# Kernel tuning notes

Measured on AMD Instinct MI355X. Metric: run time of the kernel, lower is better.

## Reference

```python
import jax, jax.numpy as jnp
import numpy as np

NEG_INF = -1e30


def setup_inputs() -> dict:
    key = jax.random.key(0)
    k1, k2, k3 = jax.random.split(key, 3)
    B, d, Lc, Lq = 64, 128, 1024, 256
    C = jax.random.normal(k1, (B, d, Lc), dtype=jnp.float32)
    Q = jax.random.normal(k2, (B, d, Lq), dtype=jnp.float32)
    cmask = jnp.ones((B, Lc), dtype=jnp.float32)
    qmask = jnp.ones((B, Lq), dtype=jnp.float32)
    # trilinear weight, uniform(-sqrt(1/d), sqrt(1/d)) as in the module init
    lim = float(np.sqrt(1.0 / d))
    w = jax.random.uniform(k3, (3 * d,), dtype=jnp.float32, minval=-lim, maxval=lim)
    return {"C": C, "Q": Q, "cmask": cmask, "qmask": qmask, "w": w}


def reference(C, Q, cmask, qmask, w):
    # C: (B, d, Lc), Q: (B, d, Lq) -> channel-last
    Ct = jnp.swapaxes(C, 1, 2)  # (B, Lc, d)
    Qt = jnp.swapaxes(Q, 1, 2)  # (B, Lq, d)
    d = Ct.shape[-1]
    w1, w2, w3 = w[:d], w[d:2 * d], w[2 * d:]
    # Decomposed trilinear score: S[b,i,j] = Ct[b,i].w1 + Qt[b,j].w2 + (Ct[b,i]*w3).Qt[b,j]
    S = (Ct @ w1)[:, :, None] + (Qt @ w2)[:, None, :] \
        + jnp.einsum('bid,bjd->bij', Ct * w3, Qt)  # (B, Lc, Lq)
    qm = qmask[:, None, :]  # (B, 1, Lq)
    cm = cmask[:, :, None]  # (B, Lc, 1)
    S1 = jax.nn.softmax(S + (1.0 - qm) * NEG_INF, axis=2)  # over query
    S2 = jax.nn.softmax(S + (1.0 - cm) * NEG_INF, axis=1)  # over context
    A = jnp.einsum('bij,bjd->bid', S1, Qt)                  # (B, Lc, d)
    Bmat = jnp.einsum('bik,bkd->bid',
                      jnp.einsum('bij,bkj->bik', S1, S2), Ct)  # (B, Lc, d)
    out = jnp.concatenate([Ct, A, Ct * A, Ct * Bmat], axis=2)  # (B, Lc, 4d)
    # dropout in eval mode (p applied only in training) -> identity
    return jnp.swapaxes(out, 1, 2)  # (B, 4d, Lc)
```

## Files before the change

kernel.cpp:

```cpp
#include <hip/hip_runtime.h>
#include <math.h>

#define B_ 64
#define D_ 128
#define LC 1024
#define LQ 256
#define NEG_INF_ (-1e30f)
#define NSPLIT 8

typedef short bf16x8 __attribute__((ext_vector_type(8)));
typedef float f32x4 __attribute__((ext_vector_type(4)));
typedef _Float16 f16x8 __attribute__((ext_vector_type(8)));
typedef _Float16 f16x4 __attribute__((ext_vector_type(4)));

__device__ __forceinline__ unsigned short bf16b(float x) {
  unsigned u = __builtin_bit_cast(unsigned, x);
  u = (u + 0x7FFFu + ((u >> 16) & 1u)) >> 16;
  return (unsigned short)u;
}

__global__ __launch_bounds__(256) void k_ca(const float* __restrict__ C,
                                            const float* __restrict__ w,
                                            float* __restrict__ ca) {
  int t = blockIdx.x * 256 + threadIdx.x;
  int b = t >> 10, i = t & (LC - 1);
  const float* Cp = C + (size_t)b * D_ * LC + i;
  float acc = 0.f;
#pragma unroll 8
  for (int dd = 0; dd < D_; ++dd) acc += Cp[(size_t)dd * LC] * w[dd];
  ca[t] = acc;
}

__global__ __launch_bounds__(256) void k_qb(const float* __restrict__ Q,
                                            const float* __restrict__ w,
                                            float* __restrict__ qb) {
  int t = blockIdx.x * 256 + threadIdx.x;
  int b = t >> 8, j = t & (LQ - 1);
  const float* Qp = Q + (size_t)b * D_ * LQ + j;
  float acc = 0.f;
#pragma unroll 8
  for (int dd = 0; dd < D_; ++dd) acc += Qp[(size_t)dd * LQ] * w[D_ + dd];
  qb[t] = acc;
}

__global__ __launch_bounds__(256) void k_qt(const float* __restrict__ Q,
                                            unsigned short* __restrict__ Qt) {
  __shared__ float ts[64][65];
  int b = blockIdx.z, d0 = blockIdx.y * 64, j0 = blockIdx.x * 64;
  int t = threadIdx.x;
  int jc = t & 15, dr = t >> 4;
#pragma unroll
  for (int ii = 0; ii < 4; ++ii) {
    int d = dr + 16 * ii;
    float4 v = *(const float4*)&Q[((size_t)b * D_ + d0 + d) * LQ + j0 + 4 * jc];
    ts[4 * jc + 0][d] = v.x;
    ts[4 * jc + 1][d] = v.y;
    ts[4 * jc + 2][d] = v.z;
    ts[4 * jc + 3][d] = v.w;
  }
  __syncthreads();
  int j = t >> 2, h = t & 3;
  unsigned short tmp[16];
#pragma unroll
  for (int k = 0; k < 16; ++k) tmp[k] = bf16b(ts[j][h * 16 + k]);
  size_t base = ((size_t)b * LQ + j0 + j) * D_ + d0 + h * 16;
  *(bf16x8*)&Qt[base] = *(bf16x8*)&tmp[0];
  *(bf16x8*)&Qt[base + 8] = *(bf16x8*)&tmp[8];
}

__global__ __launch_bounds__(256, 3) void k_S(const float* __restrict__ C,
                                              const unsigned short* __restrict__ Qt,
                                              const float* __restrict__ w,
                                              const float* __restrict__ ca,
                                              const float* __restrict__ qb,
                                              const float* __restrict__ qmask,
                                              _Float16* __restrict__ S,
                                              float* __restrict__ m1,
                                              float* __restrict__ l1) {
  __shared__ unsigned short Asw[64 * 128];
  int b = blockIdx.y;
  int i0 = blockIdx.x * 64;
  int t = threadIdx.x;
  {
    int fc = t & 15, dr = t >> 4;
#pragma unroll
    for (int ii = 0; ii < 8; ++ii) {
      int d = dr + 16 * ii;
      float w3 = w[2 * D_ + d];
      float4 v = *(const float4*)&C[((size_t)b * D_ + d) * LC + i0 + 4 * fc];
      float vv[4] = {v.x, v.y, v.z, v.w};
#pragma unroll
      for (int m = 0; m < 4; ++m) {
        int i = 4 * fc + m;
        Asw[i * 128 + (d ^ ((i & 7) << 3))] = bf16b(vv[m] * w3);
      }
    }
  }
  __syncthreads();

  int w_id = t >> 6, l = t & 63;
  int sl = l >> 4, lj = l & 15;
  int irow = w_id * 16 + lj;
  f32x4 acc[16];
#pragma unroll
  for (int jt = 0; jt < 16; ++jt) acc[jt] = (f32x4){0.f, 0.f, 0.f, 0.f};

#pragma unroll
  for (int kk = 0; kk < 4; ++kk) {
    bf16x8 af = *(const bf16x8*)&Asw[irow * 128 + ((kk * 32 + 8 * sl) ^ ((irow & 7) << 3))];
#pragma unroll
    for (int jt = 0; jt < 16; ++jt) {
      bf16x8 bf = *(const bf16x8*)&Qt[((size_t)b * LQ + jt * 16 + lj) * D_ + kk * 32 + 8 * sl];
      acc[jt] = __builtin_amdgcn_mfma_f32_16x16x32_bf16(af, bf, acc[jt], 0, 0, 0);
    }
  }

  int ibase = i0 + w_id * 16 + 4 * sl;
  float4 cav = *(const float4*)&ca[b * LC + ibase];
  float cavr[4] = {cav.x, cav.y, cav.z, cav.w};
#pragma unroll
  for (int jt = 0; jt < 16; ++jt) {
    int j = jt * 16 + lj;
    float qbv = qb[b * LQ + j];
    float qadd = (1.0f - qmask[b * LQ + j]) * NEG_INF_;
#pragma unroll
    for (int r = 0; r < 4; ++r) {
      float sval = acc[jt][r] + cavr[r] + qbv;
      S[((size_t)(b * LC + ibase + r)) * LQ + j] = (_Float16)sval;
      acc[jt][r] = sval + qadd;
    }
  }
#pragma unroll
  for (int r = 0; r < 4; ++r) {
    float m = -1e38f;
#pragma unroll
    for (int jt = 0; jt < 16; ++jt) m = fmaxf(m, acc[jt][r]);
#pragma unroll
    for (int off = 1; off <= 8; off <<= 1) m = fmaxf(m, __shfl_xor(m, off));
    float s = 0.f;
#pragma unroll
    for (int jt = 0; jt < 16; ++jt) s += __expf(acc[jt][r] - m);
#pragma unroll
    for (int off = 1; off <= 8; off <<= 1) s += __shfl_xor(s, off);
    if (lj == 0) {
      m1[b * LC + ibase + r] = m;
      l1[b * LC + ibase + r] = s;
    }
  }
}

__global__ __launch_bounds__(256) void k_colpart(const _Float16* __restrict__ S,
                                                 const float* __restrict__ cmask,
                                                 float* __restrict__ pm,
                                                 float* __restrict__ pl) {
  int split = blockIdx.x, b = blockIdx.y;
  int j = threadIdx.x;
  int ibeg = split * (LC / NSPLIT);
  float m = -1e38f, lsum = 0.f;
  for (int i = ibeg; i < ibeg + LC / NSPLIT; ++i) {
    float cm = cmask[b * LC + i];
    float v = (float)S[((size_t)b * LC + i) * LQ + j] + (1.0f - cm) * NEG_INF_;
    float nm = fmaxf(m, v);
    lsum = lsum * __expf(m - nm) + __expf(v - nm);
    m = nm;
  }
  pm[((size_t)b * NSPLIT + split) * LQ + j] = m;
  pl[((size_t)b * NSPLIT + split) * LQ + j] = lsum;
}

__global__ __launch_bounds__(256) void k_colfin(const float* __restrict__ pm,
                                                const float* __restrict__ pl,
                                                float* __restrict__ m2,
                                                float* __restrict__ l2) {
  int t = blockIdx.x * 256 + threadIdx.x;
  int b = t >> 8, j = t & (LQ - 1);
  float m = -1e38f;
#pragma unroll
  for (int s = 0; s < NSPLIT; ++s) m = fmaxf(m, pm[((size_t)b * NSPLIT + s) * LQ + j]);
  float lsum = 0.f;
#pragma unroll
  for (int s = 0; s < NSPLIT; ++s)
    lsum += pl[((size_t)b * NSPLIT + s) * LQ + j] * __expf(pm[((size_t)b * NSPLIT + s) * LQ + j] - m);
  m2[t] = m;
  l2[t] = lsum;
}

__global__ __launch_bounds__(256, 4) void k_R(const _Float16* __restrict__ S,
                                              const float* __restrict__ C,
                                              const float* __restrict__ cmask,
                                              const float* __restrict__ m2,
                                              const float* __restrict__ l2,
                                              unsigned short* __restrict__ Rt) {
  __shared__ unsigned short Pt[2][32 * 32];
  __shared__ float m2s[32], il2s[32];
  int b = blockIdx.y;
  int j0 = blockIdx.x * 32;
  int t = threadIdx.x;
  if (t < 32) {
    m2s[t] = m2[b * LQ + j0 + t];
    il2s[t] = 1.0f / l2[b * LQ + j0 + t];
  }
  __syncthreads();

  int iL = t >> 3, jc = t & 7;
  int w_id = t >> 6, l = t & 63;
  int sl = l >> 4, lj = l & 15;
  int wbase = w_id * 32;

  f32x4 acc[2][2];
#pragma unroll
  for (int dt = 0; dt < 2; ++dt)
#pragma unroll
    for (int jt = 0; jt < 2; ++jt) acc[dt][jt] = (f32x4){0.f, 0.f, 0.f, 0.f};

  {
    f16x4 sv = *(const f16x4*)&S[((size_t)(b * LC + iL)) * LQ + j0 + 4 * jc];
    float cmadd = (1.0f - cmask[b * LC + iL]) * NEG_INF_;
#pragma unroll
    for (int m = 0; m < 4; ++m) {
      int jl = 4 * jc + m;
      float p = __expf((float)sv[m] + cmadd - m2s[jl]) * il2s[jl];
      Pt[0][jl * 32 + (iL ^ ((jl & 3) << 3))] = bf16b(p);
    }
  }
  __syncthreads();

  for (int kt = 0; kt < 32; ++kt) {
    int cur = kt & 1;
    if (kt < 31) {
      int i0n = (kt + 1) * 32;
      f16x4 sv = *(const f16x4*)&S[((size_t)(b * LC + i0n + iL)) * LQ + j0 + 4 * jc];
      float cmadd = (1.0f - cmask[b * LC + i0n + iL]) * NEG_INF_;
#pragma unroll
      for (int m = 0; m < 4; ++m) {
        int jl = 4 * jc + m;
        float p = __expf((float)sv[m] + cmadd - m2s[jl]) * il2s[jl];
        Pt[cur ^ 1][jl * 32 + (iL ^ ((jl & 3) << 3))] = bf16b(p);
      }
    }
    bf16x8 af[2];
#pragma unroll
    for (int dt = 0; dt < 2; ++dt) {
      int d = wbase + dt * 16 + lj;
      const float* cp = &C[((size_t)b * D_ + d) * LC + kt * 32 + 8 * sl];
      float4 c0 = *(const float4*)cp;
      float4 c1 = *(const float4*)(cp + 4);
      unsigned short ab[8] = {bf16b(c0.x), bf16b(c0.y), bf16b(c0.z), bf16b(c0.w),
                              bf16b(c1.x), bf16b(c1.y), bf16b(c1.z), bf16b(c1.w)};
      af[dt] = *(bf16x8*)ab;
    }
#pragma unroll
    for (int jt = 0; jt < 2; ++jt) {
      bf16x8 bfp = *(const bf16x8*)&Pt[cur][(jt * 16 + lj) * 32 + ((8 * sl) ^ ((lj & 3) << 3))];
#pragma unroll
      for (int dt = 0; dt < 2; ++dt)
        acc[dt][jt] = __builtin_amdgcn_mfma_f32_16x16x32_bf16(af[dt], bfp, acc[dt][jt], 0, 0, 0);
    }
    __syncthreads();
  }

#pragma unroll
  for (int dt = 0; dt < 2; ++dt)
#pragma unroll
    for (int jt = 0; jt < 2; ++jt)
#pragma unroll
      for (int r = 0; r < 4; ++r) {
        int d = wbase + dt * 16 + 4 * sl + r;
        int j = j0 + jt * 16 + lj;
        Rt[((size_t)b * D_ + d) * LQ + j] = bf16b(acc[dt][jt][r]);
      }
}

__global__ __launch_bounds__(256, 3) void k_final(const _Float16* __restrict__ S,
                                                  const float* __restrict__ C,
                                                  const float* __restrict__ Q,
                                                  const unsigned short* __restrict__ Rt,
                                                  const float* __restrict__ qmask,
                                                  const float* __restrict__ m1,
                                                  const float* __restrict__ l1,
                                                  float* __restrict__ out) {
  __shared__ unsigned short P_lds[2][64 * 32];
  __shared__ float m1s[64], il1s[64], qadds[256];
  int b = blockIdx.y;
  int i0 = blockIdx.x * 64;
  int t = threadIdx.x;
  if (t < 64) {
    m1s[t] = m1[b * LC + i0 + t];
    il1s[t] = 1.0f / l1[b * LC + i0 + t];
  }
  qadds[t] = (1.0f - qmask[b * LQ + t]) * NEG_INF_;
  __syncthreads();

  int iL = t >> 2, jc = t & 3;
  int w_id = t >> 6, l = t & 63;
  int sl = l >> 4, lj = l & 15;
  int wbase = w_id * 32;
  float m1v = m1s[iL], il1v = il1s[iL];

  f32x4 accQ[2][4], accR[2][4];
#pragma unroll
  for (int dt = 0; dt < 2; ++dt)
#pragma unroll
    for (int it = 0; it < 4; ++it) {
      accQ[dt][it] = (f32x4){0.f, 0.f, 0.f, 0.f};
      accR[dt][it] = (f32x4){0.f, 0.f, 0.f, 0.f};
    }

  {
    f16x8 sv = *(const f16x8*)&S[((size_t)(b * LC + i0 + iL)) * LQ + 8 * jc];
    float qa[8];
    *(float4*)qa = *(const float4*)&qadds[8 * jc];
    *(float4*)(qa + 4) = *(const float4*)&qadds[8 * jc + 4];
    unsigned short pb[8];
#pragma unroll
    for (int e = 0; e < 8; ++e)
      pb[e] = bf16b(__expf((float)sv[e] + qa[e] - m1v) * il1v);
    *(bf16x8*)&P_lds[0][iL * 32 + 8 * jc] = *(bf16x8*)pb;
  }
  __syncthreads();

  for (int s = 0; s < 8; ++s) {
    int cur = s & 1;
    if (s < 7) {
      int j0n = (s + 1) * 32;
      f16x8 sv = *(const f16x8*)&S[((size_t)(b * LC + i0 + iL)) * LQ + j0n + 8 * jc];
      float qa[8];
      *(float4*)qa = *(const float4*)&qadds[j0n + 8 * jc];
      *(float4*)(qa + 4) = *(const float4*)&qadds[j0n + 8 * jc + 4];
      unsigned short pb[8];
#pragma unroll
      for (int e = 0; e < 8; ++e)
        pb[e] = bf16b(__expf((float)sv[e] + qa[e] - m1v) * il1v);
      *(bf16x8*)&P_lds[cur ^ 1][iL * 32 + 8 * jc] = *(bf16x8*)pb;
    }
    int j0c = s * 32;
    bf16x8 aQ[2], aR[2];
#pragma unroll
    for (int dt = 0; dt < 2; ++dt) {
      int d = wbase + dt * 16 + lj;
      const float* qp = &Q[((size_t)b * D_ + d) * LQ + j0c + 8 * sl];
      float4 q0 = *(const float4*)qp;
      float4 q1 = *(const float4*)(qp + 4);
      unsigned short ab[8] = {bf16b(q0.x), bf16b(q0.y), bf16b(q0.z), bf16b(q0.w),
                              bf16b(q1.x), bf16b(q1.y), bf16b(q1.z), bf16b(q1.w)};
      aQ[dt] = *(bf16x8*)ab;
      aR[dt] = *(const bf16x8*)&Rt[((size_t)b * D_ + d) * LQ + j0c + 8 * sl];
    }
#pragma unroll
    for (int it = 0; it < 4; ++it) {
      bf16x8 bP = *(const bf16x8*)&P_lds[cur][(it * 16 + lj) * 32 + 8 * sl];
#pragma unroll
      for (int dt = 0; dt < 2; ++dt) {
        accQ[dt][it] = __builtin_amdgcn_mfma_f32_16x16x32_bf16(aQ[dt], bP, accQ[dt][it], 0, 0, 0);
        accR[dt][it] = __builtin_amdgcn_mfma_f32_16x16x32_bf16(aR[dt], bP, accR[dt][it], 0, 0, 0);
      }
    }
    __syncthreads();
  }

#pragma unroll
  for (int dt = 0; dt < 2; ++dt)
#pragma unroll
    for (int it = 0; it < 4; ++it)
#pragma unroll
      for (int r = 0; r < 4; ++r) {
        int d = wbase + dt * 16 + 4 * sl + r;
        int gi = i0 + it * 16 + lj;
        float c = C[((size_t)b * D_ + d) * LC + gi];
        float a = accQ[dt][it][r];
        float bm = accR[dt][it][r];
        size_t ob = ((size_t)b * 512 + d) * LC + gi;
        out[ob] = c;
        out[ob + (size_t)128 * LC] = a;
        out[ob + (size_t)256 * LC] = c * a;
        out[ob + (size_t)384 * LC] = c * bm;
      }
}

extern "C" void kernel_launch(void* const* d_in, const int* in_sizes, int n_in,
                              void* d_out, int out_size, void* d_ws, size_t ws_size,
                              hipStream_t stream) {
  const float* C = (const float*)d_in[0];
  const float* Q = (const float*)d_in[1];
  const float* cmask = (const float*)d_in[2];
  const float* qmask = (const float*)d_in[3];
  const float* w = (const float*)d_in[4];
  float* out = (float*)d_out;
  float* ws = (float*)d_ws;

  float* ca = ws;
  float* qb = ca + (size_t)B_ * LC;
  float* m1 = qb + (size_t)B_ * LQ;
  float* l1 = m1 + (size_t)B_ * LC;
  float* m2 = l1 + (size_t)B_ * LC;
  float* l2 = m2 + (size_t)B_ * LQ;
  float* pm = l2 + (size_t)B_ * LQ;
  float* pl = pm + (size_t)B_ * NSPLIT * LQ;
  unsigned short* Qt = (unsigned short*)(pl + (size_t)B_ * NSPLIT * LQ);
  unsigned short* Rt = Qt + (size_t)B_ * LQ * D_;
  _Float16* S = (_Float16*)(Rt + (size_t)B_ * D_ * LQ);

  k_ca<<<(B_ * LC) / 256, 256, 0, stream>>>(C, w, ca);
  k_qb<<<(B_ * LQ) / 256, 256, 0, stream>>>(Q, w, qb);
  k_qt<<<dim3(LQ / 64, D_ / 64, B_), 256, 0, stream>>>(Q, Qt);
  k_S<<<dim3(LC / 64, B_), 256, 0, stream>>>(C, Qt, w, ca, qb, qmask, S, m1, l1);
  k_colpart<<<dim3(NSPLIT, B_), 256, 0, stream>>>(S, cmask, pm, pl);
  k_colfin<<<(B_ * LQ) / 256, 256, 0, stream>>>(pm, pl, m2, l2);
  k_R<<<dim3(LQ / 32, B_), 256, 0, stream>>>(S, C, cmask, m2, l2, Rt);
  k_final<<<dim3(LC / 64, B_), 256, 0, stream>>>(S, C, Q, Rt, qmask, m1, l1, out);
}
```

Baseline: 324.4 us.

## Fuse row-bias, Q prep and column softmax stats into fewer kernels

Merges the C·w1 projection into k_S, combines Q·w2 with the Q transpose into a single prep kernel, and computes per-block column max/sum statistics inside k_S from registers. The column finalisation now happens at the start of k_R. This removes four kernel launches, an extra full read of S for the column statistics, and a read of C for ca. In exchange k_S does more work, needs more shared memory and extra barriers, which could lower its occupancy.

```diff
diff --git a/kernel.cpp b/kernel.cpp
--- a/kernel.cpp
+++ b/kernel.cpp
@@ -6,7 +6,7 @@
 #define LC 1024
 #define LQ 256
 #define NEG_INF_ (-1e30f)
-#define NSPLIT 8
+#define NBLK 16
 
 typedef short bf16x8 __attribute__((ext_vector_type(8)));
 typedef float f32x4 __attribute__((ext_vector_type(4)));
@@ -19,73 +19,75 @@
   return (unsigned short)u;
 }
 
-__global__ __launch_bounds__(256) void k_ca(const float* __restrict__ C,
-                                            const float* __restrict__ w,
-                                            float* __restrict__ ca) {
-  int t = blockIdx.x * 256 + threadIdx.x;
-  int b = t >> 10, i = t & (LC - 1);
-  const float* Cp = C + (size_t)b * D_ * LC + i;
-  float acc = 0.f;
-#pragma unroll 8
-  for (int dd = 0; dd < D_; ++dd) acc += Cp[(size_t)dd * LC] * w[dd];
-  ca[t] = acc;
-}
-
-__global__ __launch_bounds__(256) void k_qb(const float* __restrict__ Q,
-                                            const float* __restrict__ w,
-                                            float* __restrict__ qb) {
-  int t = blockIdx.x * 256 + threadIdx.x;
-  int b = t >> 8, j = t & (LQ - 1);
-  const float* Qp = Q + (size_t)b * D_ * LQ + j;
-  float acc = 0.f;
-#pragma unroll 8
-  for (int dd = 0; dd < D_; ++dd) acc += Qp[(size_t)dd * LQ] * w[D_ + dd];
-  qb[t] = acc;
-}
-
-__global__ __launch_bounds__(256) void k_qt(const float* __restrict__ Q,
-                                            unsigned short* __restrict__ Qt) {
-  __shared__ float ts[64][65];
-  int b = blockIdx.z, d0 = blockIdx.y * 64, j0 = blockIdx.x * 64;
+__global__ __launch_bounds__(256) void k_prep_q(const float* __restrict__ Q,
+                                                const float* __restrict__ w,
+                                                unsigned short* __restrict__ Qt,
+                                                float* __restrict__ qb) {
+  __shared__ float ts[64][129];
+  __shared__ float qP[16][64];
+  int b = blockIdx.y, j0 = blockIdx.x * 64;
   int t = threadIdx.x;
   int jc = t & 15, dr = t >> 4;
-#pragma unroll
-  for (int ii = 0; ii < 4; ++ii) {
+  float qpart[4] = {0.f, 0.f, 0.f, 0.f};
+#pragma unroll
+  for (int ii = 0; ii < 8; ++ii) {
     int d = dr + 16 * ii;
-    float4 v = *(const float4*)&Q[((size_t)b * D_ + d0 + d) * LQ + j0 + 4 * jc];
+    float4 v = *(const float4*)&Q[((size_t)b * D_ + d) * LQ + j0 + 4 * jc];
+    float w2 = w[D_ + d];
     ts[4 * jc + 0][d] = v.x;
     ts[4 * jc + 1][d] = v.y;
     ts[4 * jc + 2][d] = v.z;
     ts[4 * jc + 3][d] = v.w;
-  }
-  __syncthreads();
+    qpart[0] += v.x * w2;
+    qpart[1] += v.y * w2;
+    qpart[2] += v.z * w2;
+    qpart[3] += v.w * w2;
+  }
+#pragma unroll
+  for (int m = 0; m < 4; ++m) qP[dr][4 * jc + m] = qpart[m];
+  __syncthreads();
+  if (t < 64) {
+    float s = 0.f;
+#pragma unroll
+    for (int r = 0; r < 16; ++r) s += qP[r][t];
+    qb[b * LQ + j0 + t] = s;
+  }
   int j = t >> 2, h = t & 3;
-  unsigned short tmp[16];
-#pragma unroll
-  for (int k = 0; k < 16; ++k) tmp[k] = bf16b(ts[j][h * 16 + k]);
-  size_t base = ((size_t)b * LQ + j0 + j) * D_ + d0 + h * 16;
-  *(bf16x8*)&Qt[base] = *(bf16x8*)&tmp[0];
-  *(bf16x8*)&Qt[base + 8] = *(bf16x8*)&tmp[8];
+  unsigned short tmp[32];
+#pragma unroll
+  for (int k = 0; k < 32; ++k) tmp[k] = bf16b(ts[j][h * 32 + k]);
+  size_t base = ((size_t)b * LQ + j0 + j) * D_ + h * 32;
+#pragma unroll
+  for (int q = 0; q < 4; ++q) *(bf16x8*)&Qt[base + 8 * q] = *(bf16x8*)&tmp[8 * q];
 }
 
 __global__ __launch_bounds__(256, 3) void k_S(const float* __restrict__ C,
                                               const unsigned short* __restrict__ Qt,
                                               const float* __restrict__ w,
-                                              const float* __restrict__ ca,
                                               const float* __restrict__ qb,
                                               const float* __restrict__ qmask,
+                                              const float* __restrict__ cmask,
                                               _Float16* __restrict__ S,
                                               float* __restrict__ m1,
-                                              float* __restrict__ l1) {
+                                              float* __restrict__ l1,
+                                              float* __restrict__ pm,
+                                              float* __restrict__ pl) {
   __shared__ unsigned short Asw[64 * 128];
+  __shared__ float caP[16][64];
+  __shared__ float ca_s[64];
+  __shared__ float qadds[256];
+  __shared__ float colM[4][256], colL[4][256];
   int b = blockIdx.y;
   int i0 = blockIdx.x * 64;
   int t = threadIdx.x;
+  qadds[t] = (1.0f - qmask[b * LQ + t]) * NEG_INF_;
   {
     int fc = t & 15, dr = t >> 4;
+    float cap[4] = {0.f, 0.f, 0.f, 0.f};
 #pragma unroll
     for (int ii = 0; ii < 8; ++ii) {
       int d = dr + 16 * ii;
+      float w1 = w[d];
       float w3 = w[2 * D_ + d];
       float4 v = *(const float4*)&C[((size_t)b * D_ + d) * LC + i0 + 4 * fc];
       float vv[4] = {v.x, v.y, v.z, v.w};
@@ -93,8 +95,18 @@
       for (int m = 0; m < 4; ++m) {
         int i = 4 * fc + m;
         Asw[i * 128 + (d ^ ((i & 7) << 3))] = bf16b(vv[m] * w3);
+        cap[m] += vv[m] * w1;
       }
     }
+#pragma unroll
+    for (int m = 0; m < 4; ++m) caP[dr][4 * fc + m] = cap[m];
+  }
+  __syncthreads();
+  if (t < 64) {
+    float s = 0.f;
+#pragma unroll
+    for (int r = 0; r < 16; ++r) s += caP[r][t];
+    ca_s[t] = s;
   }
   __syncthreads();
 
@@ -116,30 +128,29 @@
   }
 
   int ibase = i0 + w_id * 16 + 4 * sl;
-  float4 cav = *(const float4*)&ca[b * LC + ibase];
-  float cavr[4] = {cav.x, cav.y, cav.z, cav.w};
+  float cavr[4] = {ca_s[w_id * 16 + 4 * sl + 0], ca_s[w_id * 16 + 4 * sl + 1],
+                   ca_s[w_id * 16 + 4 * sl + 2], ca_s[w_id * 16 + 4 * sl + 3]};
 #pragma unroll
   for (int jt = 0; jt < 16; ++jt) {
     int j = jt * 16 + lj;
     float qbv = qb[b * LQ + j];
-    float qadd = (1.0f - qmask[b * LQ + j]) * NEG_INF_;
 #pragma unroll
     for (int r = 0; r < 4; ++r) {
       float sval = acc[jt][r] + cavr[r] + qbv;
       S[((size_t)(b * LC + ibase + r)) * LQ + j] = (_Float16)sval;
-      acc[jt][r] = sval + qadd;
+      acc[jt][r] = sval;
     }
   }
 #pragma unroll
   for (int r = 0; r < 4; ++r) {
     float m = -1e38f;
 #pragma unroll
-    for (int jt = 0; jt < 16; ++jt) m = fmaxf(m, acc[jt][r]);
+    for (int jt = 0; jt < 16; ++jt) m = fmaxf(m, acc[jt][r] + qadds[jt * 16 + lj]);
 #pragma unroll
     for (int off = 1; off <= 8; off <<= 1) m = fmaxf(m, __shfl_xor(m, off));
     float s = 0.f;
 #pragma unroll
-    for (int jt = 0; jt < 16; ++jt) s += __expf(acc[jt][r] - m);
+    for (int jt = 0; jt < 16; ++jt) s += __expf(acc[jt][r] + qadds[jt * 16 + lj] - m);
 #pragma unroll
     for (int off = 1; off <= 8; off <<= 1) s += __shfl_xor(s, off);
     if (lj == 0) {
@@ -147,49 +158,53 @@
       l1[b * LC + ibase + r] = s;
     }
   }
-}
-
-__global__ __launch_bounds__(256) void k_colpart(const _Float16* __restrict__ S,
-                                                 const float* __restrict__ cmask,
-                                                 float* __restrict__ pm,
-                                                 float* __restrict__ pl) {
-  int split = blockIdx.x, b = blockIdx.y;
-  int j = threadIdx.x;
-  int ibeg = split * (LC / NSPLIT);
-  float m = -1e38f, lsum = 0.f;
-  for (int i = ibeg; i < ibeg + LC / NSPLIT; ++i) {
-    float cm = cmask[b * LC + i];
-    float v = (float)S[((size_t)b * LC + i) * LQ + j] + (1.0f - cm) * NEG_INF_;
-    float nm = fmaxf(m, v);
-    lsum = lsum * __expf(m - nm) + __expf(v - nm);
-    m = nm;
-  }
-  pm[((size_t)b * NSPLIT + split) * LQ + j] = m;
-  pl[((size_t)b * NSPLIT + split) * LQ + j] = lsum;
-}
-
-__global__ __launch_bounds__(256) void k_colfin(const float* __restrict__ pm,
-                                                const float* __restrict__ pl,
-                                                float* __restrict__ m2,
-                                                float* __restrict__ l2) {
-  int t = blockIdx.x * 256 + threadIdx.x;
-  int b = t >> 8, j = t & (LQ - 1);
-  float m = -1e38f;
-#pragma unroll
-  for (int s = 0; s < NSPLIT; ++s) m = fmaxf(m, pm[((size_t)b * NSPLIT + s) * LQ + j]);
-  float lsum = 0.f;
-#pragma unroll
-  for (int s = 0; s < NSPLIT; ++s)
-    lsum += pl[((size_t)b * NSPLIT + s) * LQ + j] * __expf(pm[((size_t)b * NSPLIT + s) * LQ + j] - m);
-  m2[t] = m;
-  l2[t] = lsum;
+  float cmadd[4];
+#pragma unroll
+  for (int r = 0; r < 4; ++r) cmadd[r] = (1.0f - cmask[b * LC + ibase + r]) * NEG_INF_;
+#pragma unroll
+  for (int jt = 0; jt < 16; ++jt) {
+    float m = -1e38f, ls = 0.f;
+#pragma unroll
+    for (int r = 0; r < 4; ++r) {
+      float v = acc[jt][r] + cmadd[r];
+      float nm = fmaxf(m, v);
+      ls = ls * __expf(m - nm) + __expf(v - nm);
+      m = nm;
+    }
+#pragma unroll
+    for (int off = 16; off <= 32; off <<= 1) {
+      float om = __shfl_xor(m, off);
+      float ol = __shfl_xor(ls, off);
+      float nm = fmaxf(m, om);
+      ls = ls * __expf(m - nm) + ol * __expf(om - nm);
+      m = nm;
+    }
+    if (sl == 0) {
+      colM[w_id][jt * 16 + lj] = m;
+      colL[w_id][jt * 16 + lj] = ls;
+    }
+  }
+  __syncthreads();
+  {
+    int j = t;
+    float m = -1e38f, ls = 0.f;
+#pragma unroll
+    for (int wv = 0; wv < 4; ++wv) {
+      float mm = colM[wv][j], ll = colL[wv][j];
+      float nm = fmaxf(m, mm);
+      ls = ls * __expf(m - nm) + ll * __expf(mm - nm);
+      m = nm;
+    }
+    pm[((size_t)b * NBLK + blockIdx.x) * LQ + j] = m;
+    pl[((size_t)b * NBLK + blockIdx.x) * LQ + j] = ls;
+  }
 }
 
 __global__ __launch_bounds__(256, 4) void k_R(const _Float16* __restrict__ S,
                                               const float* __restrict__ C,
                                               const float* __restrict__ cmask,
-                                              const float* __restrict__ m2,
-                                              const float* __restrict__ l2,
+                                              const float* __restrict__ pm,
+                                              const float* __restrict__ pl,
                                               unsigned short* __restrict__ Rt) {
   __shared__ unsigned short Pt[2][32 * 32];
   __shared__ float m2s[32], il2s[32];
@@ -197,8 +212,17 @@
   int j0 = blockIdx.x * 32;
   int t = threadIdx.x;
   if (t < 32) {
-    m2s[t] = m2[b * LQ + j0 + t];
-    il2s[t] = 1.0f / l2[b * LQ + j0 + t];
+    float m = -1e38f, ls = 0.f;
+#pragma unroll
+    for (int s = 0; s < NBLK; ++s) {
+      float mm = pm[((size_t)b * NBLK + s) * LQ + j0 + t];
+      float ll = pl[((size_t)b * NBLK + s) * LQ + j0 + t];
+      float nm = fmaxf(m, mm);
+      ls = ls * __expf(m - nm) + ll * __expf(mm - nm);
+      m = nm;
+    }
+    m2s[t] = m;
+    il2s[t] = 1.0f / ls;
   }
   __syncthreads();
 
@@ -388,24 +412,17 @@
   float* out = (float*)d_out;
   float* ws = (float*)d_ws;
 
-  float* ca = ws;
-  float* qb = ca + (size_t)B_ * LC;
+  float* qb = ws;
   float* m1 = qb + (size_t)B_ * LQ;
   float* l1 = m1 + (size_t)B_ * LC;
-  float* m2 = l1 + (size_t)B_ * LC;
-  float* l2 = m2 + (size_t)B_ * LQ;
-  float* pm = l2 + (size_t)B_ * LQ;
-  float* pl = pm + (size_t)B_ * NSPLIT * LQ;
-  unsigned short* Qt = (unsigned short*)(pl + (size_t)B_ * NSPLIT * LQ);
+  float* pm = l1 + (size_t)B_ * LC;
+  float* pl = pm + (size_t)B_ * NBLK * LQ;
+  unsigned short* Qt = (unsigned short*)(pl + (size_t)B_ * NBLK * LQ);
   unsigned short* Rt = Qt + (size_t)B_ * LQ * D_;
   _Float16* S = (_Float16*)(Rt + (size_t)B_ * D_ * LQ);
 
-  k_ca<<<(B_ * LC) / 256, 256, 0, stream>>>(C, w, ca);
-  k_qb<<<(B_ * LQ) / 256, 256, 0, stream>>>(Q, w, qb);
-  k_qt<<<dim3(LQ / 64, D_ / 64, B_), 256, 0, stream>>>(Q, Qt);
-  k_S<<<dim3(LC / 64, B_), 256, 0, stream>>>(C, Qt, w, ca, qb, qmask, S, m1, l1);
-  k_colpart<<<dim3(NSPLIT, B_), 256, 0, stream>>>(S, cmask, pm, pl);
-  k_colfin<<<(B_ * LQ) / 256, 256, 0, stream>>>(pm, pl, m2, l2);
-  k_R<<<dim3(LQ / 32, B_), 256, 0, stream>>>(S, C, cmask, m2, l2, Rt);
+  k_prep_q<<<dim3(LQ / 64, B_), 256, 0, stream>>>(Q, w, Qt, qb);
+  k_S<<<dim3(LC / 64, B_), 256, 0, stream>>>(C, Qt, w, qb, qmask, cmask, S, m1, l1, pm, pl);
+  k_R<<<dim3(LQ / 32, B_), 256, 0, stream>>>(S, C, cmask, pm, pl, Rt);
   k_final<<<dim3(LC / 64, B_), 256, 0, stream>>>(S, C, Q, Rt, qmask, m1, l1, out);
 }
```

Result: faster. 296.1 us (-8.7%).
